# Optimization experiments

Measured on AMD Instinct MI355X. Metric: run time of the kernel, lower is better.

The kernel has to match this reference:

```python
import jax, jax.numpy as jnp
import numpy as np


def _conv(x, w, b, stride):
    # x: [B,C,H,W], w: [O,I,3,3], padding=1, given stride
    y = jax.lax.conv_general_dilated(
        x, w, window_strides=(stride, stride), padding=((1, 1), (1, 1)),
        dimension_numbers=("NCHW", "OIHW", "NCHW"))
    return y + b[None, :, None, None]


def setup_inputs() -> dict:
    key = jax.random.key(0)
    ks = jax.random.split(key, 9)
    B, H, W = 16, 256, 256
    hidden, vocab = 768, 8192
    c1, c2 = hidden // 4, hidden // 2

    def he(k, shape, fan_in):
        return jax.random.normal(k, shape, dtype=jnp.float32) * (1.0 / np.sqrt(fan_in))

    return {
        "image": jax.random.normal(ks[0], (B, 3, H, W), dtype=jnp.float32),
        "w1": he(ks[1], (c1, 3, 3, 3), 3 * 9),
        "b1": jnp.zeros((c1,), jnp.float32),
        "w2": he(ks[2], (c2, c1, 3, 3), c1 * 9),
        "b2": jnp.zeros((c2,), jnp.float32),
        "w3": he(ks[3], (hidden, c2, 3, 3), c2 * 9),
        "b3": jnp.zeros((hidden,), jnp.float32),
        "codebook": jax.random.normal(ks[4], (vocab, hidden), dtype=jnp.float32),
        "embedding_table": jax.random.normal(ks[5], (vocab, hidden), dtype=jnp.float32),
        "resolution_level": 0,
    }


def reference(image, w1, b1, w2, b2, w3, b3, codebook, embedding_table, resolution_level):
    # conv encoder: 3 -> C/4 -> C/2 -> C, each stride 2 (spatial /8)
    f = jax.nn.relu(_conv(image, w1, b1, 2))
    f = jax.nn.relu(_conv(f, w2, b2, 2))
    f = _conv(f, w3, b3, 2)                      # [B,C,H',W']
    B, C, Hp, Wp = f.shape
    feats = f.reshape(B, C, Hp * Wp).transpose(0, 2, 1)  # [B, HW, C]

    # squared euclidean distances to codebook (argmin invariant under sqrt)
    f2 = jnp.sum(feats * feats, axis=-1, keepdims=True)          # [B,HW,1]
    c2 = jnp.sum(codebook * codebook, axis=-1)                   # [V]
    d2 = f2 - 2.0 * jnp.einsum("bnc,vc->bnv", feats, codebook) + c2  # [B,HW,V]
    tokens = jnp.argmin(d2, axis=-1)                             # [B,HW] int
    embeddings = embedding_table[tokens]                         # [B,HW,C]
    return tokens, embeddings
```

## Files before the change

kernel.cpp:

```cpp
#include <hip/hip_runtime.h>
#include <hip/hip_bf16.h>
#include <float.h>


typedef __attribute__((ext_vector_type(4))) float f32x4;
typedef __attribute__((ext_vector_type(8))) _Float16 f16x8;
typedef __attribute__((ext_vector_type(8))) unsigned short u16x8;

__device__ __forceinline__ void split_f16(float x, unsigned short& hb, unsigned short& lb) {
    _Float16 h = (_Float16)x;
    _Float16 l = (_Float16)(x - (float)h);
    hb = __builtin_bit_cast(unsigned short, h);
    lb = __builtin_bit_cast(unsigned short, l);
}

__device__ __forceinline__ void gload16(const void* g, const unsigned short* l) {
    typedef unsigned int __attribute__((address_space(1))) g_u32;
    typedef unsigned int __attribute__((address_space(3))) l_u32;
    __builtin_amdgcn_global_load_lds((const g_u32*)g, (l_u32*)l, 16, 0, 0);
}

__global__ __launch_bounds__(256) void zero_kernel(unsigned short* z) {
    u16x8 v = {0, 0, 0, 0, 0, 0, 0, 0};
    *(u16x8*)&z[threadIdx.x * 8] = v;
}

__global__ __launch_bounds__(256) void reorder_w_kernel(
    const float* __restrict__ w, unsigned short* __restrict__ wh,
    unsigned short* __restrict__ wl, int COUT, int CIN)
{
    const int t = blockIdx.x * 256 + threadIdx.x;
    const int c8n = CIN / 8;
    const int total = COUT * 9 * c8n;
    if (t >= total) return;
    const int c8 = t % c8n;
    const int tap = (t / c8n) % 9;
    const int o = t / (9 * c8n);
    u16x8 vh, vl;
#pragma unroll
    for (int k = 0; k < 8; ++k) {
        const int c = c8 * 8 + k;
        unsigned short hb, lb;
        split_f16(w[((size_t)o * CIN + c) * 9 + tap], hb, lb);
        vh[k] = hb; vl[k] = lb;
    }
    const size_t dst = ((size_t)o * 9 + tap) * CIN + c8 * 8;
    *(u16x8*)&wh[dst] = vh;
    *(u16x8*)&wl[dst] = vl;
}

template <int CIN, int COUT, int HIN, int HOUT>
__global__ __launch_bounds__(256) void conv1_direct(
    const float* __restrict__ in,
    const float* __restrict__ w, const float* __restrict__ bias,
    unsigned short* __restrict__ ah, unsigned short* __restrict__ al, int nb)
{
    constexpr int WIN = HIN, WOUT = HOUT;
    constexpr int NXT = WOUT / 4;
    constexpr int NOT = COUT / 8;
    int t = blockIdx.x * 256 + threadIdx.x;
    const int total = nb * NOT * HOUT * NXT;
    if (t >= total) return;

    const int xt = t % NXT;
    const int y  = (t / NXT) % HOUT;
    int ot = (t / (NXT * HOUT)) % NOT;
    int bl = t / (NXT * HOUT * NOT);
    ot = __builtin_amdgcn_readfirstlane(ot);
    bl = __builtin_amdgcn_readfirstlane(bl);

    const int x0 = xt * 4, o0 = ot * 8;
    float acc[8][4];
#pragma unroll
    for (int i = 0; i < 8; ++i) {
        float bv = bias[o0 + i];
#pragma unroll
        for (int j = 0; j < 4; ++j) acc[i][j] = bv;
    }

    const float* inb = in + (size_t)bl * CIN * HIN * WIN;
    const float* wb  = w + (size_t)o0 * CIN * 9;

    for (int c = 0; c < CIN; ++c) {
        const float* inc = inb + (size_t)c * HIN * WIN;
#pragma unroll
        for (int ky = 0; ky < 3; ++ky) {
            const int iy = 2 * y - 1 + ky;
            if ((unsigned)iy < (unsigned)HIN) {
                const float* row = inc + (size_t)iy * WIN;
                const int sx0 = 2 * x0 - 1;
                float xin[9];
                xin[0] = (sx0 >= 0) ? row[sx0] : 0.f;
#pragma unroll
                for (int k = 1; k < 9; ++k) xin[k] = row[sx0 + k];
#pragma unroll
                for (int i = 0; i < 8; ++i) {
                    const float* wr = wb + ((size_t)i * CIN + c) * 9 + ky * 3;
                    const float w0 = wr[0], w1 = wr[1], w2 = wr[2];
#pragma unroll
                    for (int j = 0; j < 4; ++j)
                        acc[i][j] = fmaf(w0, xin[2 * j],
                                    fmaf(w1, xin[2 * j + 1],
                                    fmaf(w2, xin[2 * j + 2], acc[i][j])));
                }
            }
        }
    }

#pragma unroll
    for (int j = 0; j < 4; ++j) {
        u16x8 vh, vl;
#pragma unroll
        for (int i = 0; i < 8; ++i) {
            unsigned short hb, lb;
            split_f16(fmaxf(acc[i][j], 0.f), hb, lb);
            vh[i] = hb; vl[i] = lb;
        }
        const size_t m = (size_t)bl * (HOUT * WOUT) + (size_t)y * WOUT + x0 + j;
        *(u16x8*)&ah[m * COUT + o0] = vh;
        *(u16x8*)&al[m * COUT + o0] = vl;
    }
}

template <int CIN, int COUT, int HIN, int HOUT, int LOGW, int LOGHW, bool RELU>
__global__ __launch_bounds__(256) void conv_gemm(
    const unsigned short* __restrict__ inh, const unsigned short* __restrict__ inl,
    const unsigned short* __restrict__ wrh, const unsigned short* __restrict__ wrl,
    const float* __restrict__ bias,
    unsigned short* __restrict__ outh, unsigned short* __restrict__ outl,
    const unsigned short* __restrict__ zeros)
{
    constexpr int WIN = HIN, WOUT = HOUT;
    constexpr int KCPT = CIN / 64;
    constexpr int NSTEP = 9 * KCPT;

    __shared__ unsigned short lds[32768];
    unsigned short* As_h = lds;
    unsigned short* As_l = lds + 8192;
    unsigned short* Bs_h = lds + 16384;
    unsigned short* Bs_l = lds + 24576;

    const int tid  = threadIdx.x;
    const int lane = tid & 63;
    const int wid  = tid >> 6;
    const int ntile = blockIdx.x, mtile = blockIdx.y;
    const int m0 = mtile * 128, n0 = ntile * 128;
    const int wm = wid >> 1, wn = wid & 1;

    int aoff0[4], boff0[4], yv[4], xv[4], dstb[4];
#pragma unroll
    for (int p = 0; p < 4; ++p) {
        const int s = wid * 64 + p * 256 + lane;
        const int r = s >> 3;
        const int cl = (s & 7) ^ (r & 7);
        const int m = m0 + r;
        const int b = m >> LOGHW;
        const int y = (m >> LOGW) & (HOUT - 1);
        const int x = m & (WOUT - 1);
        yv[p] = y; xv[p] = x;
        aoff0[p] = ((b * HIN + 2 * y) * WIN + 2 * x) * CIN + cl * 8;
        boff0[p] = (n0 + r) * 9 * CIN + cl * 8;
        dstb[p] = (wid * 64 + p * 256) * 8;
    }

    f32x4 acc[4][4];
#pragma unroll
    for (int i = 0; i < 4; ++i)
#pragma unroll
        for (int j = 0; j < 4; ++j) acc[i][j] = f32x4{0.f, 0.f, 0.f, 0.f};

    for (int ks = 0; ks < NSTEP; ++ks) {
        const int tap = ks / KCPT;
        const int c0 = (ks % KCPT) * 64;
        const int ky = tap / 3, kx = tap - ky * 3;
        const int doff = ((ky - 1) * WIN + (kx - 1)) * CIN + c0;

#pragma unroll
        for (int p = 0; p < 4; ++p) {
            const bool valid = !((yv[p] == 0 && ky == 0) || (xv[p] == 0 && kx == 0));
            const unsigned short* sa_h = valid ? inh + (aoff0[p] + doff) : zeros;
            const unsigned short* sa_l = valid ? inl + (aoff0[p] + doff) : zeros;
            gload16(sa_h, As_h + dstb[p]);
            gload16(sa_l, As_l + dstb[p]);
            const int bo = boff0[p] + tap * CIN + c0;
            gload16(wrh + bo, Bs_h + dstb[p]);
            gload16(wrl + bo, Bs_l + dstb[p]);
        }
        __syncthreads();

#pragma unroll
        for (int kh = 0; kh < 2; ++kh) {
            const int cg = kh * 4 + (lane >> 4);
            f16x8 a_h[4], a_l[4], b_h[4], b_l[4];
#pragma unroll
            for (int i = 0; i < 4; ++i) {
                const int row = wm * 64 + i * 16 + (lane & 15);
                const int off = row * 64 + ((cg ^ (row & 7)) * 8);
                a_h[i] = *(const f16x8*)(As_h + off);
                a_l[i] = *(const f16x8*)(As_l + off);
            }
#pragma unroll
            for (int j = 0; j < 4; ++j) {
                const int col = wn * 64 + j * 16 + (lane & 15);
                const int off = col * 64 + ((cg ^ (col & 7)) * 8);
                b_h[j] = *(const f16x8*)(Bs_h + off);
                b_l[j] = *(const f16x8*)(Bs_l + off);
            }
#pragma unroll
            for (int i = 0; i < 4; ++i)
#pragma unroll
                for (int j = 0; j < 4; ++j) {
                    acc[i][j] = __builtin_amdgcn_mfma_f32_16x16x32_f16(
                        a_h[i], b_h[j], acc[i][j], 0, 0, 0);
                    acc[i][j] = __builtin_amdgcn_mfma_f32_16x16x32_f16(
                        a_h[i], b_l[j], acc[i][j], 0, 0, 0);
                    acc[i][j] = __builtin_amdgcn_mfma_f32_16x16x32_f16(
                        a_l[i], b_h[j], acc[i][j], 0, 0, 0);
                }
        }
        __syncthreads();
    }

    float bv4[4];
#pragma unroll
    for (int j = 0; j < 4; ++j) bv4[j] = bias[n0 + wn * 64 + j * 16 + (lane & 15)];
#pragma unroll
    for (int i = 0; i < 4; ++i)
#pragma unroll
        for (int r = 0; r < 4; ++r) {
            const size_t m = m0 + wm * 64 + i * 16 + (lane >> 4) * 4 + r;
#pragma unroll
            for (int j = 0; j < 4; ++j) {
                const int n = n0 + wn * 64 + j * 16 + (lane & 15);
                float v = acc[i][j][r] + bv4[j];
                if (RELU) v = fmaxf(v, 0.f);
                unsigned short hb, lb;
                split_f16(v, hb, lb);
                outh[m * COUT + n] = hb;
                outl[m * COUT + n] = lb;
            }
        }
}

__global__ __launch_bounds__(256) void split_codebook_kernel(
    const float* __restrict__ cb, unsigned short* __restrict__ bh,
    unsigned short* __restrict__ bl, float* __restrict__ c2)
{
    const int v = blockIdx.x * 4 + (threadIdx.x >> 6);
    const int lane = threadIdx.x & 63;
    const float* row = cb + (size_t)v * 768;
    float s = 0.f;
#pragma unroll
    for (int t = 0; t < 12; ++t) {
        const int idx = lane + 64 * t;
        float x = row[idx];
        s = fmaf(x, x, s);
        unsigned short hb, lb;
        split_f16(x, hb, lb);
        bh[(size_t)v * 768 + idx] = hb;
        bl[(size_t)v * 768 + idx] = lb;
    }
#pragma unroll
    for (int off = 32; off >= 1; off >>= 1) s += __shfl_xor(s, off, 64);
    if (lane == 0) c2[v] = s;
}

__global__ __launch_bounds__(256) void vq_mfma_kernel(
    const unsigned short* __restrict__ Ah, const unsigned short* __restrict__ Al,
    const unsigned short* __restrict__ Bh, const unsigned short* __restrict__ Bl,
    const float* __restrict__ c2,
    float* __restrict__ pval, int* __restrict__ pidx)
{
    __shared__ unsigned short lds[32768];
    unsigned short* As_h = lds;
    unsigned short* As_l = lds + 8192;
    unsigned short* Bs_h = lds + 16384;
    unsigned short* Bs_l = lds + 24576;

    const int tid  = threadIdx.x;
    const int lane = tid & 63;
    const int wid  = tid >> 6;

    const int bid    = blockIdx.x;
    const int xcd    = bid & 7;
    const int local  = bid >> 3;
    const int msuper = local >> 5;
    const int idx5   = local & 31;
    const int mtile  = msuper * 4 + (idx5 & 3);
    const int ntile  = xcd * 8 + (idx5 >> 2);

    const int m0 = mtile * 128, n0 = ntile * 128;
    const int wm = wid >> 1, wn = wid & 1;

    f32x4 acc[4][4];
#pragma unroll
    for (int i = 0; i < 4; ++i)
#pragma unroll
        for (int j = 0; j < 4; ++j) acc[i][j] = f32x4{0.f, 0.f, 0.f, 0.f};

    for (int step = 0; step < 12; ++step) {
        const int kb = step * 64;
#pragma unroll
        for (int p = 0; p < 4; ++p) {
            const int s  = wid * 64 + p * 256 + lane;
            const int r  = s >> 3;
            const int cl = (s & 7) ^ (r & 7);
            const int dstbase = (wid * 64 + p * 256) * 8;
            const size_t ga = (size_t)(m0 + r) * 768 + kb + cl * 8;
            const size_t gb = (size_t)(n0 + r) * 768 + kb + cl * 8;
            gload16(Ah + ga, As_h + dstbase);
            gload16(Al + ga, As_l + dstbase);
            gload16(Bh + gb, Bs_h + dstbase);
            gload16(Bl + gb, Bs_l + dstbase);
        }
        __syncthreads();

#pragma unroll
        for (int kh = 0; kh < 2; ++kh) {
            const int cg = kh * 4 + (lane >> 4);
            f16x8 a_h[4], a_l[4], b_h[4], b_l[4];
#pragma unroll
            for (int i = 0; i < 4; ++i) {
                const int row = wm * 64 + i * 16 + (lane & 15);
                const int off = row * 64 + ((cg ^ (row & 7)) * 8);
                a_h[i] = *(const f16x8*)(As_h + off);
                a_l[i] = *(const f16x8*)(As_l + off);
            }
#pragma unroll
            for (int j = 0; j < 4; ++j) {
                const int col = wn * 64 + j * 16 + (lane & 15);
                const int off = col * 64 + ((cg ^ (col & 7)) * 8);
                b_h[j] = *(const f16x8*)(Bs_h + off);
                b_l[j] = *(const f16x8*)(Bs_l + off);
            }
#pragma unroll
            for (int i = 0; i < 4; ++i)
#pragma unroll
                for (int j = 0; j < 4; ++j) {
                    acc[i][j] = __builtin_amdgcn_mfma_f32_16x16x32_f16(
                        a_h[i], b_h[j], acc[i][j], 0, 0, 0);
                    acc[i][j] = __builtin_amdgcn_mfma_f32_16x16x32_f16(
                        a_h[i], b_l[j], acc[i][j], 0, 0, 0);
                    acc[i][j] = __builtin_amdgcn_mfma_f32_16x16x32_f16(
                        a_l[i], b_h[j], acc[i][j], 0, 0, 0);
                }
        }
        __syncthreads();
    }

    float bestv[4][4];
    int   besti[4][4];
#pragma unroll
    for (int i = 0; i < 4; ++i)
#pragma unroll
        for (int r = 0; r < 4; ++r) { bestv[i][r] = FLT_MAX; besti[i][r] = 0; }

#pragma unroll
    for (int j = 0; j < 4; ++j) {
        const int n = n0 + wn * 64 + j * 16 + (lane & 15);
        const float cn = c2[n];
#pragma unroll
        for (int i = 0; i < 4; ++i)
#pragma unroll
            for (int r = 0; r < 4; ++r) {
                float val = fmaf(-2.f, acc[i][j][r], cn);
                if (val < bestv[i][r] || (val == bestv[i][r] && n < besti[i][r])) {
                    bestv[i][r] = val; besti[i][r] = n;
                }
            }
    }

    const int chunk = ntile * 2 + wn;
#pragma unroll
    for (int i = 0; i < 4; ++i)
#pragma unroll
        for (int r = 0; r < 4; ++r) {
            float v = bestv[i][r];
            int  ix = besti[i][r];
#pragma unroll
            for (int off = 8; off >= 1; off >>= 1) {
                float ov = __shfl_xor(v, off, 64);
                int   oi = __shfl_xor(ix, off, 64);
                if (ov < v || (ov == v && oi < ix)) { v = ov; ix = oi; }
            }
            if ((lane & 15) == 0) {
                const int m = m0 + wm * 64 + i * 16 + (lane >> 4) * 4 + r;
                pval[(size_t)chunk * 16384 + m] = v;
                pidx[(size_t)chunk * 16384 + m] = ix;
            }
        }
}

__global__ __launch_bounds__(256) void token_reduce_kernel(
    const float* __restrict__ pval, const int* __restrict__ pidx,
    float* __restrict__ tok_out)
{
    const int m = blockIdx.x * 256 + threadIdx.x;
    float bv = pval[m];
    int   bi = pidx[m];
    for (int c = 1; c < 128; ++c) {
        float v = pval[(size_t)c * 16384 + m];
        int   i = pidx[(size_t)c * 16384 + m];
        if (v < bv || (v == bv && i < bi)) { bv = v; bi = i; }
    }
    tok_out[m] = (float)bi;
}

__global__ __launch_bounds__(192) void gather_kernel(
    const float* __restrict__ tok, const float* __restrict__ table,
    float* __restrict__ emb)
{
    const int m = blockIdx.x;
    const int t = threadIdx.x;
    const int token = (int)tok[m];
    const float4* src = (const float4*)(table + (size_t)token * 768);
    float4* dst = (float4*)(emb + (size_t)m * 768);
    dst[t] = src[t];
}

extern "C" void kernel_launch(void* const* d_in, const int* in_sizes, int n_in,
                              void* d_out, int out_size, void* d_ws, size_t ws_size,
                              hipStream_t stream)
{
    const float* image = (const float*)d_in[0];
    const float* w1 = (const float*)d_in[1];
    const float* b1 = (const float*)d_in[2];
    const float* w2 = (const float*)d_in[3];
    const float* b2 = (const float*)d_in[4];
    const float* w3 = (const float*)d_in[5];
    const float* b3 = (const float*)d_in[6];
    const float* codebook = (const float*)d_in[7];
    const float* etab     = (const float*)d_in[8];

    float* out_tok = (float*)d_out;
    float* out_emb = (float*)d_out + 16384;

    char* ws = (char*)d_ws;
    unsigned short* Ah  = (unsigned short*)ws;
    unsigned short* Al  = (unsigned short*)(ws + 25165824);
    unsigned short* f1h = (unsigned short*)(ws + 50331648);
    unsigned short* f1l = (unsigned short*)(ws + 75497472);
    unsigned short* Bh  = (unsigned short*)(ws + 50331648);
    unsigned short* Bl  = (unsigned short*)(ws + 62914560);
    float* c2   = (float*)(ws + 75497472);
    float* pval = (float*)(ws + 75530240);
    int*   pidx = (int*)  (ws + 83918848);
    unsigned short* f2h = (unsigned short*)(ws + 100663296);
    unsigned short* f2l = (unsigned short*)(ws + 113246208);
    unsigned short* wr2h = (unsigned short*)(ws + 125829120);
    unsigned short* wr2l = (unsigned short*)(ws + 127156224);
    unsigned short* wr3h = (unsigned short*)(ws + 128483328);
    unsigned short* wr3l = (unsigned short*)(ws + 133791744);
    unsigned short* zeros = (unsigned short*)(ws + 139100160);

    zero_kernel<<<1, 256, 0, stream>>>(zeros);
    reorder_w_kernel<<<(384 * 9 * 24 + 255) / 256, 256, 0, stream>>>(w2, wr2h, wr2l, 384, 192);
    reorder_w_kernel<<<(768 * 9 * 48 + 255) / 256, 256, 0, stream>>>(w3, wr3h, wr3l, 768, 384);

    for (int bc = 0; bc < 4; ++bc) {
        const int b0 = bc * 4;
        const int total1 = 4 * (192 / 8) * 128 * (128 / 4);
        conv1_direct<3, 192, 256, 128>
            <<<total1 / 256, 256, 0, stream>>>(
                image + (size_t)b0 * 3 * 256 * 256, w1, b1, f1h, f1l, 4);
        conv_gemm<192, 384, 128, 64, 6, 12, true>
            <<<dim3(3, 128), 256, 0, stream>>>(
                f1h, f1l, wr2h, wr2l, b2, f2h, f2l, zeros);
        conv_gemm<384, 768, 64, 32, 5, 10, false>
            <<<dim3(6, 32), 256, 0, stream>>>(
                f2h, f2l, wr3h, wr3l, b3,
                Ah + (size_t)b0 * 1024 * 768, Al + (size_t)b0 * 1024 * 768, zeros);
    }

    split_codebook_kernel<<<2048, 256, 0, stream>>>(codebook, Bh, Bl, c2);

    vq_mfma_kernel<<<8192, 256, 0, stream>>>(Ah, Al, Bh, Bl, c2, pval, pidx);

    token_reduce_kernel<<<64, 256, 0, stream>>>(pval, pidx, out_tok);

    gather_kernel<<<16384, 192, 0, stream>>>(out_tok, etab, out_emb);
}
```

Before: 1.480 ms.

## Double-buffer LDS tiles in conv and VQ GEMMs with half-depth K steps

Both the conv implicit-GEMM and the VQ distance GEMM now split shared memory into two buffers and use a K step of 32 instead of 64. The next step's async global-to-LDS loads are issued before computing the current step, so load latency can overlap the MFMA work. The swizzle is adapted to 32-element rows. This doubles the number of steps and barriers, and each step issues less MFMA work to hide the load behind.

```diff
diff --git a/kernel.cpp b/kernel.cpp
--- a/kernel.cpp
+++ b/kernel.cpp
@@ -131,15 +131,10 @@
     const unsigned short* __restrict__ zeros)
 {
     constexpr int WIN = HIN, WOUT = HOUT;
-    constexpr int KCPT = CIN / 64;
+    constexpr int KCPT = CIN / 32;
     constexpr int NSTEP = 9 * KCPT;
 
     __shared__ unsigned short lds[32768];
-    unsigned short* As_h = lds;
-    unsigned short* As_l = lds + 8192;
-    unsigned short* Bs_h = lds + 16384;
-    unsigned short* Bs_l = lds + 24576;
-
     const int tid  = threadIdx.x;
     const int lane = tid & 63;
     const int wid  = tid >> 6;
@@ -147,12 +142,12 @@
     const int m0 = mtile * 128, n0 = ntile * 128;
     const int wm = wid >> 1, wn = wid & 1;
 
-    int aoff0[4], boff0[4], yv[4], xv[4], dstb[4];
-#pragma unroll
-    for (int p = 0; p < 4; ++p) {
+    int aoff0[2], boff0[2], yv[2], xv[2], dstb[2];
+#pragma unroll
+    for (int p = 0; p < 2; ++p) {
         const int s = wid * 64 + p * 256 + lane;
-        const int r = s >> 3;
-        const int cl = (s & 7) ^ (r & 7);
+        const int r = s >> 2;
+        const int cl = (s & 3) ^ ((r >> 1) & 3);
         const int m = m0 + r;
         const int b = m >> LOGHW;
         const int y = (m >> LOGW) & (HOUT - 1);
@@ -169,55 +164,61 @@
 #pragma unroll
         for (int j = 0; j < 4; ++j) acc[i][j] = f32x4{0.f, 0.f, 0.f, 0.f};
 
-    for (int ks = 0; ks < NSTEP; ++ks) {
+    auto STAGE = [&](int ks, unsigned short* bp) {
         const int tap = ks / KCPT;
-        const int c0 = (ks % KCPT) * 64;
+        const int c0 = (ks % KCPT) * 32;
         const int ky = tap / 3, kx = tap - ky * 3;
         const int doff = ((ky - 1) * WIN + (kx - 1)) * CIN + c0;
-
-#pragma unroll
-        for (int p = 0; p < 4; ++p) {
+#pragma unroll
+        for (int p = 0; p < 2; ++p) {
             const bool valid = !((yv[p] == 0 && ky == 0) || (xv[p] == 0 && kx == 0));
             const unsigned short* sa_h = valid ? inh + (aoff0[p] + doff) : zeros;
             const unsigned short* sa_l = valid ? inl + (aoff0[p] + doff) : zeros;
-            gload16(sa_h, As_h + dstb[p]);
-            gload16(sa_l, As_l + dstb[p]);
+            gload16(sa_h, bp + dstb[p]);
+            gload16(sa_l, bp + 4096 + dstb[p]);
             const int bo = boff0[p] + tap * CIN + c0;
-            gload16(wrh + bo, Bs_h + dstb[p]);
-            gload16(wrl + bo, Bs_l + dstb[p]);
-        }
-        __syncthreads();
-
-#pragma unroll
-        for (int kh = 0; kh < 2; ++kh) {
-            const int cg = kh * 4 + (lane >> 4);
-            f16x8 a_h[4], a_l[4], b_h[4], b_l[4];
-#pragma unroll
-            for (int i = 0; i < 4; ++i) {
-                const int row = wm * 64 + i * 16 + (lane & 15);
-                const int off = row * 64 + ((cg ^ (row & 7)) * 8);
-                a_h[i] = *(const f16x8*)(As_h + off);
-                a_l[i] = *(const f16x8*)(As_l + off);
-            }
+            gload16(wrh + bo, bp + 8192 + dstb[p]);
+            gload16(wrl + bo, bp + 12288 + dstb[p]);
+        }
+    };
+
+    auto COMPUTE = [&](const unsigned short* bp) {
+        const int cg = lane >> 4;
+        f16x8 a_h[4], a_l[4], b_h[4], b_l[4];
+#pragma unroll
+        for (int i = 0; i < 4; ++i) {
+            const int row = wm * 64 + i * 16 + (lane & 15);
+            const int off = row * 32 + ((cg ^ ((row >> 1) & 3)) * 8);
+            a_h[i] = *(const f16x8*)(bp + off);
+            a_l[i] = *(const f16x8*)(bp + 4096 + off);
+        }
+#pragma unroll
+        for (int j = 0; j < 4; ++j) {
+            const int col = wn * 64 + j * 16 + (lane & 15);
+            const int off = col * 32 + ((cg ^ ((col >> 1) & 3)) * 8);
+            b_h[j] = *(const f16x8*)(bp + 8192 + off);
+            b_l[j] = *(const f16x8*)(bp + 12288 + off);
+        }
+#pragma unroll
+        for (int i = 0; i < 4; ++i)
 #pragma unroll
             for (int j = 0; j < 4; ++j) {
-                const int col = wn * 64 + j * 16 + (lane & 15);
-                const int off = col * 64 + ((cg ^ (col & 7)) * 8);
-                b_h[j] = *(const f16x8*)(Bs_h + off);
-                b_l[j] = *(const f16x8*)(Bs_l + off);
-            }
-#pragma unroll
-            for (int i = 0; i < 4; ++i)
-#pragma unroll
-                for (int j = 0; j < 4; ++j) {
-                    acc[i][j] = __builtin_amdgcn_mfma_f32_16x16x32_f16(
-                        a_h[i], b_h[j], acc[i][j], 0, 0, 0);
-                    acc[i][j] = __builtin_amdgcn_mfma_f32_16x16x32_f16(
-                        a_h[i], b_l[j], acc[i][j], 0, 0, 0);
-                    acc[i][j] = __builtin_amdgcn_mfma_f32_16x16x32_f16(
-                        a_l[i], b_h[j], acc[i][j], 0, 0, 0);
-                }
-        }
+                acc[i][j] = __builtin_amdgcn_mfma_f32_16x16x32_f16(
+                    a_h[i], b_h[j], acc[i][j], 0, 0, 0);
+                acc[i][j] = __builtin_amdgcn_mfma_f32_16x16x32_f16(
+                    a_h[i], b_l[j], acc[i][j], 0, 0, 0);
+                acc[i][j] = __builtin_amdgcn_mfma_f32_16x16x32_f16(
+                    a_l[i], b_h[j], acc[i][j], 0, 0, 0);
+            }
+    };
+
+    STAGE(0, lds);
+    __syncthreads();
+    for (int ks = 0; ks < NSTEP; ++ks) {
+        unsigned short* cb_ = (ks & 1) ? (lds + 16384) : lds;
+        unsigned short* nb_ = (ks & 1) ? lds : (lds + 16384);
+        if (ks + 1 < NSTEP) STAGE(ks + 1, nb_);
+        COMPUTE(cb_);
         __syncthreads();
     }
 
@@ -272,11 +273,6 @@
     float* __restrict__ pval, int* __restrict__ pidx)
 {
     __shared__ unsigned short lds[32768];
-    unsigned short* As_h = lds;
-    unsigned short* As_l = lds + 8192;
-    unsigned short* Bs_h = lds + 16384;
-    unsigned short* Bs_l = lds + 24576;
-
     const int tid  = threadIdx.x;
     const int lane = tid & 63;
     const int wid  = tid >> 6;
@@ -292,59 +288,73 @@
     const int m0 = mtile * 128, n0 = ntile * 128;
     const int wm = wid >> 1, wn = wid & 1;
 
+    int rA[2], rB[2], clv[2], dstb[2];
+#pragma unroll
+    for (int p = 0; p < 2; ++p) {
+        const int s = wid * 64 + p * 256 + lane;
+        const int r = s >> 2;
+        clv[p] = (s & 3) ^ ((r >> 1) & 3);
+        rA[p] = m0 + r;
+        rB[p] = n0 + r;
+        dstb[p] = (wid * 64 + p * 256) * 8;
+    }
+
     f32x4 acc[4][4];
 #pragma unroll
     for (int i = 0; i < 4; ++i)
 #pragma unroll
         for (int j = 0; j < 4; ++j) acc[i][j] = f32x4{0.f, 0.f, 0.f, 0.f};
 
-    for (int step = 0; step < 12; ++step) {
-        const int kb = step * 64;
-#pragma unroll
-        for (int p = 0; p < 4; ++p) {
-            const int s  = wid * 64 + p * 256 + lane;
-            const int r  = s >> 3;
-            const int cl = (s & 7) ^ (r & 7);
-            const int dstbase = (wid * 64 + p * 256) * 8;
-            const size_t ga = (size_t)(m0 + r) * 768 + kb + cl * 8;
-            const size_t gb = (size_t)(n0 + r) * 768 + kb + cl * 8;
-            gload16(Ah + ga, As_h + dstbase);
-            gload16(Al + ga, As_l + dstbase);
-            gload16(Bh + gb, Bs_h + dstbase);
-            gload16(Bl + gb, Bs_l + dstbase);
-        }
-        __syncthreads();
-
-#pragma unroll
-        for (int kh = 0; kh < 2; ++kh) {
-            const int cg = kh * 4 + (lane >> 4);
-            f16x8 a_h[4], a_l[4], b_h[4], b_l[4];
-#pragma unroll
-            for (int i = 0; i < 4; ++i) {
-                const int row = wm * 64 + i * 16 + (lane & 15);
-                const int off = row * 64 + ((cg ^ (row & 7)) * 8);
-                a_h[i] = *(const f16x8*)(As_h + off);
-                a_l[i] = *(const f16x8*)(As_l + off);
-            }
+    auto STAGE = [&](int ks, unsigned short* bp) {
+        const int kb = ks * 32;
+#pragma unroll
+        for (int p = 0; p < 2; ++p) {
+            const size_t ga = (size_t)rA[p] * 768 + kb + clv[p] * 8;
+            const size_t gb = (size_t)rB[p] * 768 + kb + clv[p] * 8;
+            gload16(Ah + ga, bp + dstb[p]);
+            gload16(Al + ga, bp + 4096 + dstb[p]);
+            gload16(Bh + gb, bp + 8192 + dstb[p]);
+            gload16(Bl + gb, bp + 12288 + dstb[p]);
+        }
+    };
+
+    auto COMPUTE = [&](const unsigned short* bp) {
+        const int cg = lane >> 4;
+        f16x8 a_h[4], a_l[4], b_h[4], b_l[4];
+#pragma unroll
+        for (int i = 0; i < 4; ++i) {
+            const int row = wm * 64 + i * 16 + (lane & 15);
+            const int off = row * 32 + ((cg ^ ((row >> 1) & 3)) * 8);
+            a_h[i] = *(const f16x8*)(bp + off);
+            a_l[i] = *(const f16x8*)(bp + 4096 + off);
+        }
+#pragma unroll
+        for (int j = 0; j < 4; ++j) {
+            const int col = wn * 64 + j * 16 + (lane & 15);
+            const int off = col * 32 + ((cg ^ ((col >> 1) & 3)) * 8);
+            b_h[j] = *(const f16x8*)(bp + 8192 + off);
+            b_l[j] = *(const f16x8*)(bp + 12288 + off);
+        }
+#pragma unroll
+        for (int i = 0; i < 4; ++i)
 #pragma unroll
             for (int j = 0; j < 4; ++j) {
-                const int col = wn * 64 + j * 16 + (lane & 15);
-                const int off = col * 64 + ((cg ^ (col & 7)) * 8);
-                b_h[j] = *(const f16x8*)(Bs_h + off);
-                b_l[j] = *(const f16x8*)(Bs_l + off);
-            }
-#pragma unroll
-            for (int i = 0; i < 4; ++i)
-#pragma unroll
-                for (int j = 0; j < 4; ++j) {
-                    acc[i][j] = __builtin_amdgcn_mfma_f32_16x16x32_f16(
-                        a_h[i], b_h[j], acc[i][j], 0, 0, 0);
-                    acc[i][j] = __builtin_amdgcn_mfma_f32_16x16x32_f16(
-                        a_h[i], b_l[j], acc[i][j], 0, 0, 0);
-                    acc[i][j] = __builtin_amdgcn_mfma_f32_16x16x32_f16(
-                        a_l[i], b_h[j], acc[i][j], 0, 0, 0);
-                }
-        }
+                acc[i][j] = __builtin_amdgcn_mfma_f32_16x16x32_f16(
+                    a_h[i], b_h[j], acc[i][j], 0, 0, 0);
+                acc[i][j] = __builtin_amdgcn_mfma_f32_16x16x32_f16(
+                    a_h[i], b_l[j], acc[i][j], 0, 0, 0);
+                acc[i][j] = __builtin_amdgcn_mfma_f32_16x16x32_f16(
+                    a_l[i], b_h[j], acc[i][j], 0, 0, 0);
+            }
+    };
+
+    STAGE(0, lds);
+    __syncthreads();
+    for (int ks = 0; ks < 24; ++ks) {
+        unsigned short* cb_ = (ks & 1) ? (lds + 16384) : lds;
+        unsigned short* nb_ = (ks & 1) ? lds : (lds + 16384);
+        if (ks + 1 < 24) STAGE(ks + 1, nb_);
+        COMPUTE(cb_);
         __syncthreads();
     }
 
```

Result: slower. 1.618 ms (+9.3%).
